# Kernel optimization log

Hardware: AMD Instinct MI355X
Metric: run time of the kernel (lower is better)

The kernel has to match this reference:

```python
import jax, jax.numpy as jnp
import numpy as np

B, N, E, K, H = 4, 2048, 512, 16, 8
EMB = 2 * E  # MultiheadAttention embed_dim = input_enc * 2


def setup_inputs() -> dict:
    key = jax.random.key(0)
    ks = jax.random.split(key, 6)
    s = 0.02
    return {
        "x": jax.random.normal(ks[0], (B, N, E), jnp.float32),
        "x_enc": jax.random.normal(ks[1], (B, N, EMB), jnp.float32),
        "w_in": jax.random.normal(ks[2], (3 * EMB, EMB), jnp.float32) * s,
        "b_in": jnp.zeros((3 * EMB,), jnp.float32),
        "w_out": jax.random.normal(ks[3], (EMB, EMB), jnp.float32) * s,
        "b_out": jnp.zeros((EMB,), jnp.float32),
        "k": K,
    }


def _knn_mean(x, k):
    # x: (B, N, E). torch code transposes to (B, E, N) and treats the E channel
    # rows as the 'points' for kNN (distance matrix is (B, E, E)).
    xt = jnp.swapaxes(x, 1, 2)                      # (B, E, N)
    sq = jnp.sum(xt * xt, axis=-1)                  # (B, E)
    dist = sq[:, :, None] + sq[:, None, :] - 2.0 * jnp.einsum("ben,bfn->bef", xt, xt)
    idx = jax.lax.top_k(-dist, k)[1]                # (B, E, k) smallest distances
    # fused gather + mean: avoid the (B, E, E, N) expand from the torch code
    nbrs = jnp.take_along_axis(xt[:, None, :, :], idx[:, :, :, None], axis=2)  # (B, E, k, N)
    return jnp.swapaxes(jnp.mean(nbrs, axis=2), 1, 2)  # (B, N, E)


def _mha(q, kv, w_in, b_in, w_out, b_out, h):
    # faithful torch nn.MultiheadAttention (batch_first) forward
    wq, wk, wv = jnp.split(w_in, 3, axis=0)
    bq, bk, bv = jnp.split(b_in, 3, axis=0)
    Q = q @ wq.T + bq
    Kt = kv @ wk.T + bk
    V = kv @ wv.T + bv
    b, l, emb = Q.shape
    m = Kt.shape[1]
    d = emb // h

    def split_heads(t):
        return t.reshape(t.shape[0], t.shape[1], h, d).transpose(0, 2, 1, 3)

    Qh, Kh, Vh = split_heads(Q), split_heads(Kt), split_heads(V)
    scores = jnp.einsum("bhld,bhmd->bhlm", Qh, Kh) / jnp.sqrt(jnp.float32(d))
    att = jax.nn.softmax(scores, axis=-1)
    o = jnp.einsum("bhlm,bhmd->bhld", att, Vh)      # (B, H, L, d)
    o = o.transpose(0, 2, 1, 3).reshape(b, l, emb)
    return o @ w_out.T + b_out


def reference(x, x_enc, w_in, b_in, w_out, b_out, k):
    b, n, e = x.shape
    x_knn = _knn_mean(x, k)                          # (B, N, E)
    cat = jnp.concatenate([jnp.swapaxes(x, 1, 2), jnp.swapaxes(x_knn, 1, 2)], axis=-1)  # (B, E, 2N)
    # faithful to torch .view(-1, 2*E, N): row-interleaving reshape, NOT a transpose
    q = jnp.swapaxes(cat.reshape(b, 2 * e, n), 1, 2)  # (B, N, 2E)
    attn = _mha(q, x_enc, w_in, b_in, w_out, b_out, H)  # (B, N, 2E)
    return jnp.concatenate([q, attn], axis=1)         # (B, 2N, 2E)
```

## Files before the change

kernel.cpp:

```cpp
#include <hip/hip_runtime.h>
#include <hip/hip_bf16.h>

#define B_ 4
#define N_ 2048
#define E_ 512
#define EMB_ 1024
#define H_ 8
#define D_ 128
#define KNN_ 16

typedef short short8_t __attribute__((ext_vector_type(8)));
typedef short short4_t __attribute__((ext_vector_type(4)));
typedef float float2_t __attribute__((ext_vector_type(2)));
typedef float float4_t __attribute__((ext_vector_type(4)));
typedef float float16_t __attribute__((ext_vector_type(16)));
typedef unsigned int uint2_t __attribute__((ext_vector_type(2)));
typedef unsigned int uint4_t __attribute__((ext_vector_type(4)));

__device__ __forceinline__ short f2bf(float f) {
  unsigned u = __float_as_uint(f);
  unsigned r = u + 0x7fffu + ((u >> 16) & 1u);
  return (short)(r >> 16);
}

__device__ __forceinline__ unsigned pk2bf(float a, float b) {
  float2 f; f.x = a; f.y = b;
  __hip_bfloat162 h = __float22bfloat162_rn(f);
  return *(unsigned*)&h;
}

__device__ __forceinline__ float fexp2(float x) {
  return __builtin_amdgcn_exp2f(x);
}

__device__ __forceinline__ void gload16(const short* g, short* l) {
  __builtin_amdgcn_global_load_lds(
      (const __attribute__((address_space(1))) void*)g,
      (__attribute__((address_space(3))) void*)l, 16, 0, 0);
}

__global__ __launch_bounds__(256) void k_sqnp_part(const float* __restrict__ x,
                                                   float* __restrict__ part) {
  const int t = blockIdx.x * 256 + threadIdx.x;
  if (t >= B_ * E_ * 16) return;
  const int be = t & (B_ * E_ - 1), blk = t >> 11;
  const int b = be >> 9, e = be & (E_ - 1);
  const float* p = x + (size_t)b * N_ * E_ + (size_t)blk * 128 * E_ + e;
  float lane[16];
#pragma unroll
  for (int l = 0; l < 16; l++) {
    float pr[8];
#pragma unroll
    for (int j = 0; j < 8; j++) {
      float v = p[(size_t)(j * 16 + l) * E_];
      pr[j] = __fmul_rn(v, v);
    }
    float s01 = __fadd_rn(pr[0], pr[1]);
    float s23 = __fadd_rn(pr[2], pr[3]);
    float s45 = __fadd_rn(pr[4], pr[5]);
    float s67 = __fadd_rn(pr[6], pr[7]);
    lane[l] = __fadd_rn(__fadd_rn(s01, s23), __fadd_rn(s45, s67));
  }
  float bb[8];
#pragma unroll
  for (int l = 0; l < 8; l++) bb[l] = __fadd_rn(lane[l], lane[l + 8]);
  float cc[4];
#pragma unroll
  for (int l = 0; l < 4; l++) cc[l] = __fadd_rn(bb[l], bb[l + 4]);
  part[(size_t)be * 16 + blk] =
      __fadd_rn(__fadd_rn(cc[0], cc[1]), __fadd_rn(cc[2], cc[3]));
}

__global__ __launch_bounds__(256) void k_sqnp_fin(const float* __restrict__ part,
                                                  float* __restrict__ sq) {
  const int t = blockIdx.x * 256 + threadIdx.x;
  if (t >= B_ * E_) return;
  const float* bs = part + (size_t)t * 16;
  float t1[8], t2[4];
#pragma unroll
  for (int l = 0; l < 8; l++) t1[l] = __fadd_rn(bs[2 * l], bs[2 * l + 1]);
#pragma unroll
  for (int l = 0; l < 4; l++) t2[l] = __fadd_rn(t1[2 * l], t1[2 * l + 1]);
  sq[t] = __fadd_rn(__fadd_rn(t2[0], t2[1]), __fadd_rn(t2[2], t2[3]));
}

__global__ __launch_bounds__(64) void k_gram_sym(const float* __restrict__ x,
                                                 float* __restrict__ g) {
  __shared__ __align__(16) float Xs[2][32][68];
  const int bx = blockIdx.x;
  int p = bx >> 1;
  const int jh = bx & 1;
  const int b = blockIdx.y;
  int ti = 0;
  while (p >= 16 - ti) { p -= 16 - ti; ti++; }
  const int tj = ti + p;
  const int i0 = ti * 32, j0 = tj * 32 + jh * 16;
  const int lane = threadIdx.x;
  const int li = lane & 7, lj = lane >> 3;
  const int cq = lane & 7, rn = lane >> 3;
  const int qj = lane & 3, rj = lane >> 2;
  const float* xb = x + (size_t)b * N_ * E_;

  float acc[4][2];
#pragma unroll
  for (int u = 0; u < 4; u++) { acc[u][0] = 0.f; acc[u][1] = 0.f; }

  float4_t gi[4], gj[2];
#pragma unroll
  for (int ps = 0; ps < 4; ps++) {
    const int n = ps * 8 + rn;
    gi[ps] = *(const float4_t*)(xb + (size_t)n * E_ + i0 + cq * 4);
  }
#pragma unroll
  for (int s = 0; s < 2; s++) {
    const int n = s * 16 + rj;
    gj[s] = *(const float4_t*)(xb + (size_t)n * E_ + j0 + qj * 4);
  }
#pragma unroll
  for (int ps = 0; ps < 4; ps++) {
    const int nn = ps * 8 + rn;
    *(float4_t*)&Xs[0][nn][(cq * 4) ^ ((nn & 7) << 2)] = gi[ps];
  }
#pragma unroll
  for (int s = 0; s < 2; s++) {
    const int nn = s * 16 + rj;
    *(float4_t*)&Xs[0][nn][32 + ((qj * 4) ^ ((nn & 3) << 2))] = gj[s];
  }

  for (int c = 0; c < 64; c++) {
    const int buf = c & 1;
    if (c < 63) {
      const int nb = (c + 1) * 32;
#pragma unroll
      for (int ps = 0; ps < 4; ps++) {
        const int n = nb + ps * 8 + rn;
        gi[ps] = *(const float4_t*)(xb + (size_t)n * E_ + i0 + cq * 4);
      }
#pragma unroll
      for (int s = 0; s < 2; s++) {
        const int n = nb + s * 16 + rj;
        gj[s] = *(const float4_t*)(xb + (size_t)n * E_ + j0 + qj * 4);
      }
    }
#pragma unroll
    for (int nn = 0; nn < 32; nn++) {
      const float4_t va = *(const float4_t*)
          &Xs[buf][nn][(li * 4) ^ ((nn & 7) << 2)];
      const float2_t vb = *(const float2_t*)
          &Xs[buf][nn][32 + (((lj >> 1) * 4) ^ ((nn & 3) << 2)) + (lj & 1) * 2];
#pragma unroll
      for (int u = 0; u < 4; u++) {
        acc[u][0] = __fadd_rn(acc[u][0], __fmul_rn(va[u], vb[0]));
        acc[u][1] = __fadd_rn(acc[u][1], __fmul_rn(va[u], vb[1]));
      }
    }
    if (c < 63) {
#pragma unroll
      for (int ps = 0; ps < 4; ps++) {
        const int nn = ps * 8 + rn;
        *(float4_t*)&Xs[buf ^ 1][nn][(cq * 4) ^ ((nn & 7) << 2)] = gi[ps];
      }
#pragma unroll
      for (int s = 0; s < 2; s++) {
        const int nn = s * 16 + rj;
        *(float4_t*)&Xs[buf ^ 1][nn][32 + ((qj * 4) ^ ((nn & 3) << 2))] = gj[s];
      }
    }
  }
  float* gb = g + (size_t)b * E_ * E_;
#pragma unroll
  for (int u = 0; u < 4; u++) {
#pragma unroll
    for (int v = 0; v < 2; v++) {
      const int i = i0 + li * 4 + u, j = j0 + lj * 2 + v;
      gb[(size_t)i * E_ + j] = acc[u][v];
      if (ti != tj) gb[(size_t)j * E_ + i] = acc[u][v];
    }
  }
}

__global__ __launch_bounds__(64) void k_topk(const float* __restrict__ sq,
                                             const float* __restrict__ g,
                                             int* __restrict__ idxout) {
  const int bi = blockIdx.x;
  const int b = bi >> 9, i = bi & (E_ - 1);
  const int lane = threadIdx.x;
  const float* gb = g + ((size_t)b * E_ + i) * E_;
  const float* sqb = sq + ((size_t)b << 9);
  const float sqi = sqb[i];
  const int base = lane * 8;
  float v[8];
#pragma unroll
  for (int u = 0; u < 8; u++) {
    v[u] = __fsub_rn(__fadd_rn(sqi, sqb[base + u]),
                     __fmul_rn(2.0f, gb[base + u]));
  }
  for (int t = 0; t < KNN_; t++) {
    float best = 3.0e38f; int bidx = E_;
#pragma unroll
    for (int u = 0; u < 8; u++) {
      if (v[u] < best) { best = v[u]; bidx = base + u; }
    }
#pragma unroll
    for (int off = 1; off < 64; off <<= 1) {
      float ov = __shfl_xor(best, off);
      int oi = __shfl_xor(bidx, off);
      if (ov < best || (ov == best && oi < bidx)) { best = ov; bidx = oi; }
    }
    if (lane == 0) idxout[(size_t)bi * KNN_ + t] = bidx;
#pragma unroll
    for (int u = 0; u < 8; u++) {
      if (bidx == base + u) v[u] = 3.0e38f;
    }
  }
}

__global__ __launch_bounds__(256) void k_knnmean(const float* __restrict__ x,
                                                 const int* __restrict__ idx,
                                                 float* __restrict__ out,
                                                 short* __restrict__ Xq) {
  const int n = blockIdx.x, b = blockIdx.y;
  const int tid = threadIdx.x;
  __shared__ float xrow[E_];
  const float* xr = x + ((size_t)b * N_ + n) * E_;
  for (int i = tid; i < E_; i += 256) xrow[i] = xr[i];
  __syncthreads();
  float* orow = out + ((size_t)b * (2 * N_) + n) * EMB_;
  unsigned* qrow = (unsigned*)(Xq + ((size_t)b * N_ + n) * EMB_);
  for (int i = tid; i < E_; i += 256) {
    const int* id = idx + ((size_t)b * E_ + i) * KNN_;
    float s = 0.f;
#pragma unroll
    for (int t = 0; t < KNN_; t++) s = __fadd_rn(s, xrow[id[t]]);
    float2 w; w.x = xrow[i]; w.y = s * (1.0f / 16.0f);
    *(float2*)&orow[2 * i] = w;
    qrow[i] = pk2bf(w.x, w.y);
  }
}

__global__ __launch_bounds__(256) void k_cvt(const float* __restrict__ src,
                                             short* __restrict__ dst, int n8) {
  const int t = blockIdx.x * 256 + threadIdx.x;
  if (t >= n8) return;
  const float* s = src + (size_t)t * 8;
  float4 a = *(const float4*)s, b = *(const float4*)(s + 4);
  short8_t v;
  v[0] = f2bf(a.x); v[1] = f2bf(a.y); v[2] = f2bf(a.z); v[3] = f2bf(a.w);
  v[4] = f2bf(b.x); v[5] = f2bf(b.y); v[6] = f2bf(b.z); v[7] = f2bf(b.w);
  *(short8_t*)(dst + (size_t)t * 8) = v;
}

__global__ __launch_bounds__(256) void k_gemm_qkv(
    const short* __restrict__ Xq, const short* __restrict__ Xe,
    const short* __restrict__ Win, const float* __restrict__ b_in,
    short* __restrict__ Qb, short* __restrict__ Kb, short* __restrict__ Vb) {
  __shared__ __align__(16) short As[128 * 64];
  __shared__ __align__(16) short Bs[128 * 64];
  const int tid = threadIdx.x;
  const int z = blockIdx.z;
  const short* X = (z == 0) ? Xq : Xe;
  const short* W = Win + (size_t)z * EMB_ * EMB_;
  const float* bias = b_in + z * EMB_;
  const int row0 = blockIdx.x * 128, col0 = blockIdx.y * 128;
  const int l = tid & 63, lg = l >> 4, lq = l & 15;
  const int w = tid >> 6, wm = w >> 1, wn = w & 1;
  float4_t acc[4][4];
#pragma unroll
  for (int i = 0; i < 4; i++)
#pragma unroll
    for (int j = 0; j < 4; j++) {
      acc[i][j][0] = 0.f; acc[i][j][1] = 0.f; acc[i][j][2] = 0.f; acc[i][j][3] = 0.f;
    }

  int soff[4], ldsb[4];
#pragma unroll
  for (int ii = 0; ii < 4; ii++) {
    const int cid = ii * 256 + tid;
    const int r = cid >> 3, c = cid & 7;
    soff[ii] = r * EMB_ + ((c * 8) ^ ((r & 7) << 3));
    ldsb[ii] = (ii * 256 + w * 64) * 8;
  }
  const short* Xb = X + (size_t)row0 * EMB_;
  const short* Wb = W + (size_t)col0 * EMB_;

  for (int kt = 0; kt < 16; kt++) {
    __syncthreads();
#pragma unroll
    for (int ii = 0; ii < 4; ii++) {
      gload16(Xb + soff[ii] + kt * 64, As + ldsb[ii]);
      gload16(Wb + soff[ii] + kt * 64, Bs + ldsb[ii]);
    }
    __syncthreads();
#pragma unroll
    for (int kk = 0; kk < 2; kk++) {
      short8_t af[4], bf[4];
#pragma unroll
      for (int mi = 0; mi < 4; mi++) {
        const int r = wm * 64 + mi * 16 + lq;
        af[mi] = *(const short8_t*)&As[r * 64 + ((kk * 32 + lg * 8) ^ ((r & 7) << 3))];
      }
#pragma unroll
      for (int ni = 0; ni < 4; ni++) {
        const int r = wn * 64 + ni * 16 + lq;
        bf[ni] = *(const short8_t*)&Bs[r * 64 + ((kk * 32 + lg * 8) ^ ((r & 7) << 3))];
      }
#pragma unroll
      for (int mi = 0; mi < 4; mi++)
#pragma unroll
        for (int ni = 0; ni < 4; ni++)
          acc[mi][ni] = __builtin_amdgcn_mfma_f32_16x16x32_bf16(af[mi], bf[ni], acc[mi][ni], 0, 0, 0);
    }
  }
  short* Yb = (z == 0) ? Qb : ((z == 1) ? Kb : Vb);
#pragma unroll
  for (int ni = 0; ni < 4; ni++) {
    const int col = col0 + wn * 64 + ni * 16 + lq;
    const float bv = bias[col];
#pragma unroll
    for (int mi = 0; mi < 4; mi++) {
#pragma unroll
      for (int j = 0; j < 4; j++) {
        const int m = row0 + wm * 64 + mi * 16 + lg * 4 + j;
        const float v = acc[mi][ni][j] + bv;
        if (z < 2) {
          Yb[(size_t)m * EMB_ + col] = f2bf(v);
        } else {
          const int b2 = m >> 11, n2 = m & (N_ - 1);
          Yb[((size_t)b2 * EMB_ + col) * N_ + n2] = f2bf(v);
        }
      }
    }
  }
}

__global__ __launch_bounds__(256) void k_gemm_out(
    const short* __restrict__ X, const short* __restrict__ W,
    const float* __restrict__ bias, float* __restrict__ Yf) {
  __shared__ __align__(16) short As[128 * 64];
  __shared__ __align__(16) short Bs[128 * 64];
  const int tid = threadIdx.x;
  const int row0 = blockIdx.x * 128, col0 = blockIdx.y * 128;
  const int l = tid & 63, lg = l >> 4, lq = l & 15;
  const int w = tid >> 6, wm = w >> 1, wn = w & 1;
  float4_t acc[4][4];
#pragma unroll
  for (int i = 0; i < 4; i++)
#pragma unroll
    for (int j = 0; j < 4; j++) {
      acc[i][j][0] = 0.f; acc[i][j][1] = 0.f; acc[i][j][2] = 0.f; acc[i][j][3] = 0.f;
    }

  int soff[4], ldsb[4];
#pragma unroll
  for (int ii = 0; ii < 4; ii++) {
    const int cid = ii * 256 + tid;
    const int r = cid >> 3, c = cid & 7;
    soff[ii] = r * EMB_ + ((c * 8) ^ ((r & 7) << 3));
    ldsb[ii] = (ii * 256 + w * 64) * 8;
  }
  const short* Xb = X + (size_t)row0 * EMB_;
  const short* Wb = W + (size_t)col0 * EMB_;

  for (int kt = 0; kt < 16; kt++) {
    __syncthreads();
#pragma unroll
    for (int ii = 0; ii < 4; ii++) {
      gload16(Xb + soff[ii] + kt * 64, As + ldsb[ii]);
      gload16(Wb + soff[ii] + kt * 64, Bs + ldsb[ii]);
    }
    __syncthreads();
#pragma unroll
    for (int kk = 0; kk < 2; kk++) {
      short8_t af[4], bf[4];
#pragma unroll
      for (int mi = 0; mi < 4; mi++) {
        const int r = wm * 64 + mi * 16 + lq;
        af[mi] = *(const short8_t*)&As[r * 64 + ((kk * 32 + lg * 8) ^ ((r & 7) << 3))];
      }
#pragma unroll
      for (int ni = 0; ni < 4; ni++) {
        const int r = wn * 64 + ni * 16 + lq;
        bf[ni] = *(const short8_t*)&Bs[r * 64 + ((kk * 32 + lg * 8) ^ ((r & 7) << 3))];
      }
#pragma unroll
      for (int mi = 0; mi < 4; mi++)
#pragma unroll
        for (int ni = 0; ni < 4; ni++)
          acc[mi][ni] = __builtin_amdgcn_mfma_f32_16x16x32_bf16(af[mi], bf[ni], acc[mi][ni], 0, 0, 0);
    }
  }
#pragma unroll
  for (int ni = 0; ni < 4; ni++) {
    const int col = col0 + wn * 64 + ni * 16 + lq;
    const float bv = bias[col];
#pragma unroll
    for (int mi = 0; mi < 4; mi++) {
#pragma unroll
      for (int j = 0; j < 4; j++) {
        const int m = row0 + wm * 64 + mi * 16 + lg * 4 + j;
        const int b2 = m >> 11, n2 = m & (N_ - 1);
        Yf[((size_t)b2 * 2 * N_ + N_ + n2) * EMB_ + col] = acc[mi][ni][j] + bv;
      }
    }
  }
}

__global__ __launch_bounds__(256, 2) void k_flash_bf16(
    const short* __restrict__ Qg, const short* __restrict__ Kg,
    const short* __restrict__ Vtg, short* __restrict__ Og) {
  __shared__ __align__(16) short Ks[2][64 * 128];
  __shared__ __align__(16) short Vs[2][128 * 64];
  const int tid = threadIdx.x;
  const int w = tid >> 6, l = tid & 63;
  const int hi = l >> 5, l5 = l & 31;
  const int bid = blockIdx.x;
  const int bh = (bid & 7) * 4 + ((bid >> 3) >> 4);
  const int rt = (bid >> 3) & 15;
  const int b = bh >> 3, h = bh & 7;
  const float c1 = 0.08838834764831845f * 1.4426950408889634f;
  const size_t bhoff = (size_t)b * N_ * EMB_ + (size_t)h * D_;
  const int ksw = (l5 & 15) << 3;
  const int psw = (l5 & 7) << 3;

  int ksrc[4], vsrc[4], ldb[4];
#pragma unroll
  for (int ii = 0; ii < 4; ii++) {
    const int cid = ii * 256 + tid;
    const int kr = cid >> 4, kc = cid & 15;
    const int vr = cid >> 3, vc = cid & 7;
    ksrc[ii] = kr * EMB_ + ((kc * 8) ^ ((kr & 15) << 3));
    vsrc[ii] = vr * N_ + ((vc * 8) ^ ((vr & 7) << 3));
    ldb[ii] = (ii * 256 + w * 64) * 8;
  }
  const short* Kt0 = Kg + bhoff;
  const short* Vt0 = Vtg + (size_t)b * EMB_ * N_ + (size_t)(h * D_) * N_;

  short8_t qf[8];
  {
    const short* qrow = Qg + bhoff + (size_t)(rt * 128 + w * 32 + l5) * EMB_;
#pragma unroll
    for (int s = 0; s < 8; s++)
      qf[s] = *(const short8_t*)(qrow + s * 16 + hi * 8);
  }
  float16_t oacc[4];
#pragma unroll
  for (int dg = 0; dg < 4; dg++)
#pragma unroll
    for (int r = 0; r < 16; r++) oacc[dg][r] = 0.f;
  float m = -3.0e38f, lsum = 0.f;

#pragma unroll
  for (int ii = 0; ii < 4; ii++) {
    gload16(Kt0 + ksrc[ii], &Ks[0][ldb[ii]]);
    gload16(Vt0 + vsrc[ii], &Vs[0][ldb[ii]]);
  }
  __syncthreads();

  for (int kt = 0; kt < N_ / 64; kt++) {
    const int buf = kt & 1;
    if (kt + 1 < N_ / 64) {
      const short* Kt = Kt0 + (size_t)((kt + 1) * 64) * EMB_;
      const short* Vt = Vt0 + (kt + 1) * 64;
#pragma unroll
      for (int ii = 0; ii < 4; ii++) {
        gload16(Kt + ksrc[ii], &Ks[buf ^ 1][ldb[ii]]);
        gload16(Vt + vsrc[ii], &Vs[buf ^ 1][ldb[ii]]);
      }
    }

    float16_t s0, s1;
#pragma unroll
    for (int r = 0; r < 16; r++) { s0[r] = 0.f; s1[r] = 0.f; }
    __builtin_amdgcn_s_setprio(1);
#pragma unroll
    for (int s = 0; s < 8; s++) {
      const int col = (s * 16 + hi * 8) ^ ksw;
      short8_t kf0 = *(const short8_t*)&Ks[buf][l5 * 128 + col];
      short8_t kf1 = *(const short8_t*)&Ks[buf][(32 + l5) * 128 + col];
      s0 = __builtin_amdgcn_mfma_f32_32x32x16_bf16(kf0, qf[s], s0, 0, 0, 0);
      s1 = __builtin_amdgcn_mfma_f32_32x32x16_bf16(kf1, qf[s], s1, 0, 0, 0);
    }
    __builtin_amdgcn_s_setprio(0);

    float tm = s0[0];
#pragma unroll
    for (int r = 1; r < 16; r++) tm = fmaxf(tm, s0[r]);
#pragma unroll
    for (int r = 0; r < 16; r++) tm = fmaxf(tm, s1[r]);
    tm = fmaxf(tm, __shfl_xor(tm, 32));
    if (__any(tm > m + 62.7f)) {
      const float mn = fmaxf(m, tm);
      const float alpha = fexp2((m - mn) * c1);
      m = mn;
      lsum *= alpha;
#pragma unroll
      for (int dg = 0; dg < 4; dg++)
#pragma unroll
        for (int r = 0; r < 16; r++) oacc[dg][r] *= alpha;
    }
    const float mc1 = m * c1;
    float ps = 0.f;
    unsigned w0[8], w1[8];
#pragma unroll
    for (int t = 0; t < 4; t++) {
      float p0 = fexp2(__builtin_fmaf(s0[4 * t + 0], c1, -mc1));
      float p1 = fexp2(__builtin_fmaf(s0[4 * t + 1], c1, -mc1));
      float p2 = fexp2(__builtin_fmaf(s0[4 * t + 2], c1, -mc1));
      float p3 = fexp2(__builtin_fmaf(s0[4 * t + 3], c1, -mc1));
      ps += (p0 + p1) + (p2 + p3);
      w0[t] = pk2bf(p0, p1); w1[t] = pk2bf(p2, p3);
    }
#pragma unroll
    for (int t = 0; t < 4; t++) {
      float p0 = fexp2(__builtin_fmaf(s1[4 * t + 0], c1, -mc1));
      float p1 = fexp2(__builtin_fmaf(s1[4 * t + 1], c1, -mc1));
      float p2 = fexp2(__builtin_fmaf(s1[4 * t + 2], c1, -mc1));
      float p3 = fexp2(__builtin_fmaf(s1[4 * t + 3], c1, -mc1));
      ps += (p0 + p1) + (p2 + p3);
      w0[4 + t] = pk2bf(p0, p1); w1[4 + t] = pk2bf(p2, p3);
    }
    ps += __shfl_xor(ps, 32);
    lsum += ps;

    short8_t pf[4];
#pragma unroll
    for (int ks = 0; ks < 4; ks++) {
      const int t0 = 2 * ks, t1 = 2 * ks + 1;
      uint2_t ra = __builtin_amdgcn_permlane32_swap(w0[t0], w0[t1], false, false);
      uint2_t rb = __builtin_amdgcn_permlane32_swap(w1[t0], w1[t1], false, false);
      uint4_t pw; pw[0] = ra[0]; pw[1] = rb[0]; pw[2] = ra[1]; pw[3] = rb[1];
      pf[ks] = *(short8_t*)&pw;
    }

    __builtin_amdgcn_s_setprio(1);
#pragma unroll
    for (int ks = 0; ks < 4; ks++) {
      const int col = (ks * 16 + hi * 8) ^ psw;
#pragma unroll
      for (int dg = 0; dg < 4; dg++) {
        short8_t vf = *(const short8_t*)&Vs[buf][(dg * 32 + l5) * 64 + col];
        oacc[dg] = __builtin_amdgcn_mfma_f32_32x32x16_bf16(vf, pf[ks], oacc[dg], 0, 0, 0);
      }
    }
    __builtin_amdgcn_s_setprio(0);

    __syncthreads();
  }

  const float linv = 1.0f / lsum;
  short* orow = Og + bhoff + (size_t)(rt * 128 + w * 32 + l5) * EMB_;
#pragma unroll
  for (int dg = 0; dg < 4; dg++) {
#pragma unroll
    for (int g = 0; g < 4; g++) {
      float p0 = oacc[dg][4 * g + 0] * linv;
      float p1 = oacc[dg][4 * g + 1] * linv;
      float p2 = oacc[dg][4 * g + 2] * linv;
      float p3 = oacc[dg][4 * g + 3] * linv;
      uint2 ow; ow.x = pk2bf(p0, p1); ow.y = pk2bf(p2, p3);
      *(uint2*)&orow[dg * 32 + g * 8 + hi * 4] = ow;
    }
  }
}

extern "C" void kernel_launch(void* const* d_in, const int* in_sizes, int n_in,
                              void* d_out, int out_size, void* d_ws, size_t ws_size,
                              hipStream_t stream) {
  const float* x     = (const float*)d_in[0];
  const float* x_enc = (const float*)d_in[1];
  const float* w_in  = (const float*)d_in[2];
  const float* b_in  = (const float*)d_in[3];
  const float* w_out = (const float*)d_in[4];
  const float* b_out = (const float*)d_in[5];
  float* out = (float*)d_out;
  char* wsb = (char*)d_ws;

  const size_t oG    = 0;
  const size_t oSq   = oG + (size_t)B_ * E_ * E_ * 4;
  const size_t oPart = oSq + (size_t)B_ * E_ * 4;
  const size_t oIdx  = oPart + (size_t)B_ * E_ * 16 * 4;
  const size_t oXq   = (oIdx + (size_t)B_ * E_ * KNN_ * 4 + 255) & ~(size_t)255;
  const size_t sB    = (size_t)B_ * N_ * EMB_ * 2;
  const size_t oXe   = oXq + sB;
  const size_t oWin  = oXe + sB;
  const size_t oWo   = oWin + 3ull * EMB_ * EMB_ * 2;
  const size_t oQ    = oWo + (size_t)EMB_ * EMB_ * 2;
  const size_t oK    = oQ + sB;
  const size_t oV    = oK + sB;
  const size_t oO    = oV + sB;
  const size_t need  = oO + sB;

  float* g    = (float*)(wsb + oG);
  float* sqv  = (float*)(wsb + oSq);
  float* part = (float*)(wsb + oPart);
  int*   idx  = (int*)(wsb + oIdx);
  short* Xq   = (short*)(wsb + oXq);
  short* Xe   = (short*)(wsb + oXe);
  short* Win  = (short*)(wsb + oWin);
  short* Wo   = (short*)(wsb + oWo);
  short* Qb   = (short*)(wsb + oQ);
  short* Kb   = (short*)(wsb + oK);
  short* Vb   = (short*)(wsb + oV);
  short* Ob   = (ws_size >= need) ? (short*)(wsb + oO) : Qb;

  k_sqnp_part<<<dim3(B_ * E_ * 16 / 256), 256, 0, stream>>>(x, part);
  k_sqnp_fin<<<dim3(B_ * E_ / 256), 256, 0, stream>>>(part, sqv);
  k_gram_sym<<<dim3(272, B_), 64, 0, stream>>>(x, g);
  k_topk<<<dim3(B_ * E_), 64, 0, stream>>>(sqv, g, idx);
  k_knnmean<<<dim3(N_, B_), 256, 0, stream>>>(x, idx, out, Xq);

  k_cvt<<<dim3(4096), 256, 0, stream>>>(x_enc, Xe, B_ * N_ * EMB_ / 8);
  k_cvt<<<dim3(1536), 256, 0, stream>>>(w_in, Win, 3 * EMB_ * EMB_ / 8);
  k_cvt<<<dim3(512), 256, 0, stream>>>(w_out, Wo, EMB_ * EMB_ / 8);

  k_gemm_qkv<<<dim3(64, 8, 3), 256, 0, stream>>>(Xq, Xe, Win, b_in, Qb, Kb, Vb);

  k_flash_bf16<<<dim3(512), 256, 0, stream>>>(Qb, Kb, Vb, Ob);

  k_gemm_out<<<dim3(64, 8), 256, 0, stream>>>(Ob, Wo, b_out, out);
}
```

Baseline: 324.2 us.

## Merge small kNN-prep and conversion kernels to cut launches; tree-reduce softmax max/sum

Folds the squared-norm partial kernel into the Gram kernel as extra blocks, and moves the final 16-way norm reduction into topk. Each topk block recomputes the norms from the partials, which adds redundant loads and adds. The three bf16 conversion kernels become one launch. In the flash kernel, the row-max and exp-sum reductions are rewritten as trees to shorten dependency chains. The main aim is to remove three to four launch gaps and let the norm work run alongside the Gram tiles.

```diff
diff --git a/kernel.cpp b/kernel.cpp
--- a/kernel.cpp
+++ b/kernel.cpp
@@ -39,58 +39,52 @@
       (__attribute__((address_space(3))) void*)l, 16, 0, 0);
 }
 
-__global__ __launch_bounds__(256) void k_sqnp_part(const float* __restrict__ x,
-                                                   float* __restrict__ part) {
-  const int t = blockIdx.x * 256 + threadIdx.x;
-  if (t >= B_ * E_ * 16) return;
-  const int be = t & (B_ * E_ - 1), blk = t >> 11;
-  const int b = be >> 9, e = be & (E_ - 1);
-  const float* p = x + (size_t)b * N_ * E_ + (size_t)blk * 128 * E_ + e;
-  float lane[16];
-#pragma unroll
-  for (int l = 0; l < 16; l++) {
-    float pr[8];
-#pragma unroll
-    for (int j = 0; j < 8; j++) {
-      float v = p[(size_t)(j * 16 + l) * E_];
-      pr[j] = __fmul_rn(v, v);
-    }
-    float s01 = __fadd_rn(pr[0], pr[1]);
-    float s23 = __fadd_rn(pr[2], pr[3]);
-    float s45 = __fadd_rn(pr[4], pr[5]);
-    float s67 = __fadd_rn(pr[6], pr[7]);
-    lane[l] = __fadd_rn(__fadd_rn(s01, s23), __fadd_rn(s45, s67));
-  }
-  float bb[8];
-#pragma unroll
-  for (int l = 0; l < 8; l++) bb[l] = __fadd_rn(lane[l], lane[l + 8]);
-  float cc[4];
-#pragma unroll
-  for (int l = 0; l < 4; l++) cc[l] = __fadd_rn(bb[l], bb[l + 4]);
-  part[(size_t)be * 16 + blk] =
-      __fadd_rn(__fadd_rn(cc[0], cc[1]), __fadd_rn(cc[2], cc[3]));
-}
-
-__global__ __launch_bounds__(256) void k_sqnp_fin(const float* __restrict__ part,
-                                                  float* __restrict__ sq) {
-  const int t = blockIdx.x * 256 + threadIdx.x;
-  if (t >= B_ * E_) return;
-  const float* bs = part + (size_t)t * 16;
+__device__ __forceinline__ float tree16(const float* __restrict__ bs) {
   float t1[8], t2[4];
 #pragma unroll
   for (int l = 0; l < 8; l++) t1[l] = __fadd_rn(bs[2 * l], bs[2 * l + 1]);
 #pragma unroll
   for (int l = 0; l < 4; l++) t2[l] = __fadd_rn(t1[2 * l], t1[2 * l + 1]);
-  sq[t] = __fadd_rn(__fadd_rn(t2[0], t2[1]), __fadd_rn(t2[2], t2[3]));
-}
-
-__global__ __launch_bounds__(64) void k_gram_sym(const float* __restrict__ x,
-                                                 float* __restrict__ g) {
+  return __fadd_rn(__fadd_rn(t2[0], t2[1]), __fadd_rn(t2[2], t2[3]));
+}
+
+__global__ __launch_bounds__(64) void k_gram_sqnp(const float* __restrict__ x,
+                                                  float* __restrict__ g,
+                                                  float* __restrict__ part) {
+  const int bx = blockIdx.x;
+  const int b = blockIdx.y;
+  if (bx >= 272) {
+    const int idx = (bx - 272) * 64 + threadIdx.x;
+    const int e = idx & (E_ - 1), blk = idx >> 9;
+    const float* p = x + (size_t)b * N_ * E_ + (size_t)blk * 128 * E_ + e;
+    float lane[16];
+#pragma unroll
+    for (int l = 0; l < 16; l++) {
+      float pr[8];
+#pragma unroll
+      for (int j = 0; j < 8; j++) {
+        float v = p[(size_t)(j * 16 + l) * E_];
+        pr[j] = __fmul_rn(v, v);
+      }
+      float s01 = __fadd_rn(pr[0], pr[1]);
+      float s23 = __fadd_rn(pr[2], pr[3]);
+      float s45 = __fadd_rn(pr[4], pr[5]);
+      float s67 = __fadd_rn(pr[6], pr[7]);
+      lane[l] = __fadd_rn(__fadd_rn(s01, s23), __fadd_rn(s45, s67));
+    }
+    float bb[8];
+#pragma unroll
+    for (int l = 0; l < 8; l++) bb[l] = __fadd_rn(lane[l], lane[l + 8]);
+    float cc[4];
+#pragma unroll
+    for (int l = 0; l < 4; l++) cc[l] = __fadd_rn(bb[l], bb[l + 4]);
+    part[((size_t)b * E_ + e) * 16 + blk] =
+        __fadd_rn(__fadd_rn(cc[0], cc[1]), __fadd_rn(cc[2], cc[3]));
+    return;
+  }
   __shared__ __align__(16) float Xs[2][32][68];
-  const int bx = blockIdx.x;
   int p = bx >> 1;
   const int jh = bx & 1;
-  const int b = blockIdx.y;
   int ti = 0;
   while (p >= 16 - ti) { p -= 16 - ti; ti++; }
   const int tj = ti + p;
@@ -179,21 +173,21 @@
   }
 }
 
-__global__ __launch_bounds__(64) void k_topk(const float* __restrict__ sq,
+__global__ __launch_bounds__(64) void k_topk(const float* __restrict__ part,
                                              const float* __restrict__ g,
                                              int* __restrict__ idxout) {
   const int bi = blockIdx.x;
   const int b = bi >> 9, i = bi & (E_ - 1);
   const int lane = threadIdx.x;
   const float* gb = g + ((size_t)b * E_ + i) * E_;
-  const float* sqb = sq + ((size_t)b << 9);
-  const float sqi = sqb[i];
+  const float* pb = part + ((size_t)b << 9) * 16;
+  const float sqi = tree16(pb + (size_t)i * 16);
   const int base = lane * 8;
   float v[8];
 #pragma unroll
   for (int u = 0; u < 8; u++) {
-    v[u] = __fsub_rn(__fadd_rn(sqi, sqb[base + u]),
-                     __fmul_rn(2.0f, gb[base + u]));
+    const float sqj = tree16(pb + (size_t)(base + u) * 16);
+    v[u] = __fsub_rn(__fadd_rn(sqi, sqj), __fmul_rn(2.0f, gb[base + u]));
   }
   for (int t = 0; t < KNN_; t++) {
     float best = 3.0e38f; int bidx = E_;
@@ -238,16 +232,25 @@
   }
 }
 
-__global__ __launch_bounds__(256) void k_cvt(const float* __restrict__ src,
-                                             short* __restrict__ dst, int n8) {
-  const int t = blockIdx.x * 256 + threadIdx.x;
-  if (t >= n8) return;
-  const float* s = src + (size_t)t * 8;
-  float4 a = *(const float4*)s, b = *(const float4*)(s + 4);
+__global__ __launch_bounds__(256) void k_cvt3(const float* __restrict__ xe,
+                                              const float* __restrict__ wi,
+                                              const float* __restrict__ wo,
+                                              short* __restrict__ Xe,
+                                              short* __restrict__ Wi,
+                                              short* __restrict__ Wo) {
+  const size_t t = (size_t)blockIdx.x * 256 + threadIdx.x;
+  const float* src; short* dst;
+  if (t < 1048576u) { src = xe + t * 8; dst = Xe + t * 8; }
+  else if (t < 1048576u + 393216u) {
+    const size_t r = t - 1048576u; src = wi + r * 8; dst = Wi + r * 8;
+  } else {
+    const size_t r = t - 1441792u; src = wo + r * 8; dst = Wo + r * 8;
+  }
+  float4 a = *(const float4*)src, b = *(const float4*)(src + 4);
   short8_t v;
   v[0] = f2bf(a.x); v[1] = f2bf(a.y); v[2] = f2bf(a.z); v[3] = f2bf(a.w);
   v[4] = f2bf(b.x); v[5] = f2bf(b.y); v[6] = f2bf(b.z); v[7] = f2bf(b.w);
-  *(short8_t*)(dst + (size_t)t * 8) = v;
+  *(short8_t*)dst = v;
 }
 
 __global__ __launch_bounds__(256) void k_gemm_qkv(
@@ -482,11 +485,14 @@
     }
     __builtin_amdgcn_s_setprio(0);
 
-    float tm = s0[0];
-#pragma unroll
-    for (int r = 1; r < 16; r++) tm = fmaxf(tm, s0[r]);
-#pragma unroll
-    for (int r = 0; r < 16; r++) tm = fmaxf(tm, s1[r]);
+    float t8[8];
+#pragma unroll
+    for (int r = 0; r < 8; r++)
+      t8[r] = fmaxf(fmaxf(s0[2 * r], s0[2 * r + 1]),
+                    fmaxf(s1[2 * r], s1[2 * r + 1]));
+    float t4a = fmaxf(t8[0], t8[1]), t4b = fmaxf(t8[2], t8[3]);
+    float t4c = fmaxf(t8[4], t8[5]), t4d = fmaxf(t8[6], t8[7]);
+    float tm = fmaxf(fmaxf(t4a, t4b), fmaxf(t4c, t4d));
     tm = fmaxf(tm, __shfl_xor(tm, 32));
     if (__any(tm > m + 62.7f)) {
       const float mn = fmaxf(m, tm);
@@ -499,7 +505,7 @@
         for (int r = 0; r < 16; r++) oacc[dg][r] *= alpha;
     }
     const float mc1 = m * c1;
-    float ps = 0.f;
+    float psg[8];
     unsigned w0[8], w1[8];
 #pragma unroll
     for (int t = 0; t < 4; t++) {
@@ -507,7 +513,7 @@
       float p1 = fexp2(__builtin_fmaf(s0[4 * t + 1], c1, -mc1));
       float p2 = fexp2(__builtin_fmaf(s0[4 * t + 2], c1, -mc1));
       float p3 = fexp2(__builtin_fmaf(s0[4 * t + 3], c1, -mc1));
-      ps += (p0 + p1) + (p2 + p3);
+      psg[t] = (p0 + p1) + (p2 + p3);
       w0[t] = pk2bf(p0, p1); w1[t] = pk2bf(p2, p3);
     }
 #pragma unroll
@@ -516,9 +522,11 @@
       float p1 = fexp2(__builtin_fmaf(s1[4 * t + 1], c1, -mc1));
       float p2 = fexp2(__builtin_fmaf(s1[4 * t + 2], c1, -mc1));
       float p3 = fexp2(__builtin_fmaf(s1[4 * t + 3], c1, -mc1));
-      ps += (p0 + p1) + (p2 + p3);
+      psg[4 + t] = (p0 + p1) + (p2 + p3);
       w0[4 + t] = pk2bf(p0, p1); w1[4 + t] = pk2bf(p2, p3);
     }
+    float ps = ((psg[0] + psg[1]) + (psg[2] + psg[3])) +
+               ((psg[4] + psg[5]) + (psg[6] + psg[7]));
     ps += __shfl_xor(ps, 32);
     lsum += ps;
 
@@ -591,7 +599,6 @@
   const size_t need  = oO + sB;
 
   float* g    = (float*)(wsb + oG);
-  float* sqv  = (float*)(wsb + oSq);
   float* part = (float*)(wsb + oPart);
   int*   idx  = (int*)(wsb + oIdx);
   short* Xq   = (short*)(wsb + oXq);
@@ -603,15 +610,11 @@
   short* Vb   = (short*)(wsb + oV);
   short* Ob   = (ws_size >= need) ? (short*)(wsb + oO) : Qb;
 
-  k_sqnp_part<<<dim3(B_ * E_ * 16 / 256), 256, 0, stream>>>(x, part);
-  k_sqnp_fin<<<dim3(B_ * E_ / 256), 256, 0, stream>>>(part, sqv);
-  k_gram_sym<<<dim3(272, B_), 64, 0, stream>>>(x, g);
-  k_topk<<<dim3(B_ * E_), 64, 0, stream>>>(sqv, g, idx);
+  k_gram_sqnp<<<dim3(400, B_), 64, 0, stream>>>(x, g, part);
+  k_topk<<<dim3(B_ * E_), 64, 0, stream>>>(part, g, idx);
   k_knnmean<<<dim3(N_, B_), 256, 0, stream>>>(x, idx, out, Xq);
 
-  k_cvt<<<dim3(4096), 256, 0, stream>>>(x_enc, Xe, B_ * N_ * EMB_ / 8);
-  k_cvt<<<dim3(1536), 256, 0, stream>>>(w_in, Win, 3 * EMB_ * EMB_ / 8);
-  k_cvt<<<dim3(512), 256, 0, stream>>>(w_out, Wo, EMB_ * EMB_ / 8);
+  k_cvt3<<<dim3(6144), 256, 0, stream>>>(x_enc, w_in, w_out, Xe, Win, Wo);
 
   k_gemm_qkv<<<dim3(64, 8, 3), 256, 0, stream>>>(Xq, Xe, Win, b_in, Qb, Kb, Vb);
 
```

Measured after the change: 323.0 us. No clear change (-0.4%).
